# Performance work log

Measured on AMD Instinct MI355X. Metric: run time of the kernel, lower is better.

The kernel has to match this reference:

```python
import jax, jax.numpy as jnp
import numpy as np

B, C, N = 1, 128, 8192
K, KNN, RES, NUM, NUM_LEVELS, BASE_SCALE = 128, 32, 3, 27, 3, 0.25


def _prelu(x, a):
    return jnp.where(x >= 0, x, a.reshape(()) * x)


def _gn(x, gamma, beta, groups, eps=1e-5):
    b, ch = x.shape[0], x.shape[1]
    xr = x.reshape(b, groups, -1)
    mu = xr.mean(axis=2, keepdims=True)
    var = xr.var(axis=2, keepdims=True)
    xn = ((xr - mu) * jax.lax.rsqrt(var + eps)).reshape(x.shape)
    shp = (1, ch) + (1,) * (x.ndim - 2)
    return xn * gamma.reshape(shp) + beta.reshape(shp)


def _conv1x1(x, W, b):
    y = jnp.einsum('oc,bc...->bo...', W, x)
    return y + b.reshape((1, -1) + (1,) * (x.ndim - 2))


def _base():
    i = np.arange(NUM)
    return jnp.asarray(np.stack([i // 9 % 3 - 1, i // 3 % 3 - 1, i % 3 - 1], 1).astype(np.float32))


def _forward(fmap1, fmap2, xyz2, coords,
             out_w1, out_b1, out_g, out_bt, out_pr, out_w2, out_b2,
             vox_w1, vox_b1, vox_g, vox_bt, vox_pr, vox_w2, vox_b2,
             knn_w1, knn_b1, knn_g, knn_bt, knn_pr, knn_ow, knn_ob):
    b, c, n_p = fmap1.shape
    sg = jax.lax.stop_gradient
    # correlation + truncation (init_module)
    corr = jnp.einsum('bcn,bcm->bnm', fmap1, fmap2) / jnp.sqrt(jnp.asarray(c, fmap1.dtype))
    tcorr, tidx = jax.lax.top_k(corr, K)                       # (b, n_p, K)
    bi = jnp.arange(b)[:, None, None]
    ni = jnp.arange(n_p)[None, :, None]
    txyz2 = xyz2[bi, tidx]                                     # (b, n_p, K, 3)
    ones = jnp.ones_like(tcorr)

    feats = []
    # multi-level voxel average pooling (scatter_add into 27 cubes)
    for i in range(NUM_LEVELS):
        r = BASE_SCALE * 2 ** i
        dv = jnp.round((txyz2 - coords[:, :, None, :]) / r)
        valid = jnp.all(jnp.abs(dv) <= 1.0, axis=-1)
        iv = dv + 1.0
        cube = (iv[..., 0] * 9 + iv[..., 1] * 3 + iv[..., 2]).astype(jnp.int32)
        cube = sg(jnp.where(valid, cube, 0))
        vf = sg(valid.astype(tcorr.dtype))
        cadd = jnp.zeros((b, n_p, NUM), tcorr.dtype).at[bi, ni, cube].add(tcorr * vf)
        ccnt = jnp.clip(jnp.zeros((b, n_p, NUM), tcorr.dtype).at[bi, ni, cube].add(ones * vf), 1, n_p)
        feats.append((cadd / ccnt).transpose(0, 2, 1))         # (b, 27, n_p)

    # coarse level: scatter_max to find per-cube center candidates (all no-grad)
    r = BASE_SCALE * 2 ** 3
    R = 2.0 * r
    sxyz, scrd = sg(txyz2), sg(coords)
    dv = jnp.round((sxyz - scrd[:, :, None, :]) / R)
    validc = jnp.all(jnp.abs(dv) <= 1.5, axis=-1)
    cidx = ((dv[..., 0] + 1.0) * 9 + (dv[..., 1] + 1.0) * 3 + (dv[..., 2] + 1.0)).astype(jnp.int32) + 1
    cidx = jnp.where(validc, cidx, 0)                          # (b, n_p, K) in [0, 27]
    vals = sg(tcorr) * validc
    masked = jnp.where(cidx[..., None] == jnp.arange(NUM + 1), vals[..., None], -jnp.inf)
    center_corr = masked.max(axis=2)[:, :, 1:]                 # (b, n_p, 27)
    center_idx = masked.argmax(axis=2)[:, :, 1:]
    mask_oob = center_corr <= 0                                # covers empty bins (-inf)
    center_idx = jnp.where(mask_oob, 0, center_idx)
    center_coord = sxyz[bi, ni, center_idx]                    # (b, n_p, 27, 3)

    base = _base()
    lim = (R - r) / 2.0
    idx_scatter = jnp.full((b, n_p, K), NUM, jnp.int32)
    moves = []
    for k in range(NUM):                                       # fixed 27-voxel loop
        vkc = (scrd + base[k] * R)[:, :, None, :]
        mv = jnp.clip(center_coord[:, :, k:k + 1, :] - vkc, -lim, lim) + vkc
        moves.append(mv)
        rep = jnp.all(jnp.abs((sxyz - mv) / r) <= 0.5, axis=-1) & ~mask_oob[:, :, k:k + 1]
        idx_scatter = jnp.where(rep, k, idx_scatter)           # later k overwrites (torch order)
    voxel_xyz = jnp.concatenate(moves, axis=2)                 # (b, n_p, 27, 3), no-grad

    cadd = jnp.zeros((b, n_p, NUM + 1), tcorr.dtype).at[bi, ni, idx_scatter].add(tcorr)
    ccnt = jnp.zeros((b, n_p, NUM + 1), tcorr.dtype).at[bi, ni, idx_scatter].add(ones)
    voxel_corr = cadd[:, :, :NUM] / jnp.clip(ccnt[:, :, :NUM], 1, n_p)

    vin = jnp.concatenate([voxel_corr[:, None], voxel_xyz.transpose(0, 3, 1, 2)], axis=1)  # (b,4,n_p,27)
    h = _prelu(_gn(_conv1x1(vin, vox_w1, vox_b1), vox_g, vox_bt, 8), vox_pr)
    h = _conv1x1(h, vox_w2, vox_b2)                            # (b,1,n_p,27)
    feats.append(h[:, 0].transpose(0, 2, 1))                   # (b,27,n_p)

    vfeat = jnp.concatenate(feats, axis=1)                     # (b,108,n_p)
    vfeat = _prelu(_gn(_conv1x1(vfeat, out_w1, out_b1), out_g, out_bt, 8), out_pr)
    voxel_out = _conv1x1(vfeat, out_w2, out_b2)                # (b,64,n_p)

    # knn branch
    dist = jnp.sum((txyz2 - coords[:, :, None, :]) ** 2, axis=-1)
    _, nbr = jax.lax.top_k(-sg(dist), KNN)                     # (b,n_p,KNN)
    knn_corr = jnp.take_along_axis(tcorr, nbr, axis=2)[:, None]            # (b,1,n_p,KNN)
    knn_xyz = txyz2[bi, ni, nbr].transpose(0, 3, 1, 2) - coords.transpose(0, 2, 1)[:, :, :, None]
    kf = _prelu(_gn(_conv1x1(jnp.concatenate([knn_corr, knn_xyz], 1), knn_w1, knn_b1), knn_g, knn_bt, 8), knn_pr)
    kf = kf.max(axis=3)                                        # (b,64,n_p)
    return voxel_out + _conv1x1(kf, knn_ow, knn_ob)


def setup_inputs() -> dict:
    key = jax.random.key(0)
    ks = jax.random.split(key, 26)
    xyz2 = jax.random.uniform(ks[0], (B, N, 3), jnp.float32, -3.0, 3.0)
    coords = xyz2 + 0.3 * jax.random.normal(ks[1], (B, N, 3), jnp.float32)
    w = lambda k, s, sc=0.1: sc * jax.random.normal(k, s, jnp.float32)
    return {
        'fmap1': jax.random.normal(ks[2], (B, C, N), jnp.float32),
        'fmap2': jax.random.normal(ks[3], (B, C, N), jnp.float32),
        'xyz2': xyz2, 'coords': coords,
        'out_w1': w(ks[4], (128, 108)), 'out_b1': w(ks[5], (128,)),
        'out_g': 1.0 + w(ks[6], (128,), 0.05), 'out_bt': w(ks[7], (128,), 0.05),
        'out_pr': jnp.full((1,), 0.25, jnp.float32),
        'out_w2': w(ks[8], (64, 128)), 'out_b2': w(ks[9], (64,)),
        'vox_w1': w(ks[10], (32, 4)), 'vox_b1': w(ks[11], (32,)),
        'vox_g': 1.0 + w(ks[12], (32,), 0.05), 'vox_bt': w(ks[13], (32,), 0.05),
        'vox_pr': jnp.full((1,), 0.25, jnp.float32),
        'vox_w2': w(ks[14], (1, 32)), 'vox_b2': w(ks[15], (1,)),
        'knn_w1': w(ks[16], (64, 4)), 'knn_b1': w(ks[17], (64,)),
        'knn_g': 1.0 + w(ks[18], (64,), 0.05), 'knn_bt': w(ks[19], (64,), 0.05),
        'knn_pr': jnp.full((1,), 0.25, jnp.float32),
        'knn_ow': w(ks[20], (64, 64)), 'knn_ob': w(ks[21], (64,)),
    }


def reference(fmap1, fmap2, xyz2, coords,
              out_w1, out_b1, out_g, out_bt, out_pr, out_w2, out_b2,
              vox_w1, vox_b1, vox_g, vox_bt, vox_pr, vox_w2, vox_b2,
              knn_w1, knn_b1, knn_g, knn_bt, knn_pr, knn_ow, knn_ob):
    return _forward(fmap1, fmap2, xyz2, coords,
                    out_w1, out_b1, out_g, out_bt, out_pr, out_w2, out_b2,
                    vox_w1, vox_b1, vox_g, vox_bt, vox_pr, vox_w2, vox_b2,
                    knn_w1, knn_b1, knn_g, knn_bt, knn_pr, knn_ow, knn_ob)
```

## Files before the change

kernel.cpp:

```cpp
#include <hip/hip_runtime.h>
#include <math.h>

#define NPT 8192
#define CCH 128
#define KK  128

typedef __attribute__((ext_vector_type(8))) short short8;
typedef __attribute__((ext_vector_type(4))) float f32x4;

__device__ __forceinline__ unsigned f2key(float f) {
  unsigned u = __float_as_uint(f);
  return u ^ ((u & 0x80000000u) ? 0xFFFFFFFFu : 0x80000000u);
}
__device__ __forceinline__ float key2f(unsigned k) {
  unsigned u = (k & 0x80000000u) ? (k ^ 0x80000000u) : ~k;
  return __uint_as_float(u);
}

__global__ void k_zero(double* s) {
  int t = threadIdx.x;
  if (t < 76) s[t] = 0.0;
}

__global__ __launch_bounds__(256) void k_split(const float* __restrict__ src,
                                               short* __restrict__ d0,
                                               short* __restrict__ d1,
                                               short* __restrict__ d2) {
  __shared__ float tile[2048];
  int g = blockIdx.x, t = threadIdx.x;
#pragma unroll
  for (int p = 0; p < 8; ++p) {
    int i = t + p * 256;
    int c = i >> 4, m = i & 15;
    tile[i] = src[(size_t)c * NPT + g * 16 + m];
  }
  __syncthreads();
  int o = t >> 4, m = t & 15;
  short8 w0, w1, w2;
#pragma unroll
  for (int j = 0; j < 8; ++j) {
    float a = tile[(o * 8 + j) * 16 + m];
    unsigned ua = __float_as_uint(a);
    unsigned uh = ua & 0xFFFF0000u;
    float r = a - __uint_as_float(uh);
    unsigned um = __float_as_uint(r) & 0xFFFF0000u;
    float r2 = r - __uint_as_float(um);
    unsigned ul = __float_as_uint(r2) & 0xFFFF0000u;
    w0[j] = (short)(uh >> 16);
    w1[j] = (short)(um >> 16);
    w2[j] = (short)(ul >> 16);
  }
  size_t base = (((size_t)g * 16 + o) * 16 + m) * 8;
  *(short8*)(d0 + base) = w0;
  *(short8*)(d1 + base) = w1;
  *(short8*)(d2 + base) = w2;
}

#define BHALF 12288
__global__ __launch_bounds__(256) void k_gemm_mfma(
    const short* __restrict__ a0, const short* __restrict__ a1, const short* __restrict__ a2,
    const short* __restrict__ b0, const short* __restrict__ b1, const short* __restrict__ b2,
    unsigned short* __restrict__ kslab, unsigned short* __restrict__ rslab, int row0) {
  __shared__ short bl[2 * BHALF];
  int tid = threadIdx.x;
  int wv = tid >> 6, lane = tid & 63;
  int m15 = lane & 15, quad = lane >> 4;
  int rowgb = (row0 >> 4) + blockIdx.y * 8 + wv * 2;
  int colg0 = blockIdx.x * 8;
  int bu_t[6], bu_oc[6], bu_m[6], bu_split[6], bu_laddr[6];
#pragma unroll
  for (int k = 0; k < 6; ++k) {
    int u = tid + k * 256;
    bu_split[k] = u >> 9;
    int r1 = u & 511;
    bu_t[k] = r1 >> 6;
    bu_oc[k] = (r1 >> 4) & 3;
    bu_m[k] = r1 & 15;
    bu_laddr[k] = (((bu_split[k] * 8 + bu_t[k]) * 4 + bu_oc[k]) * 16 + bu_m[k]) * 8;
  }
  f32x4 acc[2][8];
#pragma unroll
  for (int rg = 0; rg < 2; ++rg)
#pragma unroll
    for (int t = 0; t < 8; ++t) acc[rg][t] = (f32x4){0.f, 0.f, 0.f, 0.f};
  {
    short8 bv[6];
#pragma unroll
    for (int k = 0; k < 6; ++k) {
      const short* bp = (bu_split[k] == 0) ? b0 : (bu_split[k] == 1) ? b1 : b2;
      size_t gaddr = (((size_t)(colg0 + bu_t[k]) * 16 + (0 * 4 + bu_oc[k])) * 16 + bu_m[k]) * 8;
      bv[k] = *(const short8*)(bp + gaddr);
    }
#pragma unroll
    for (int k = 0; k < 6; ++k) *(short8*)(bl + bu_laddr[k]) = bv[k];
  }
  __syncthreads();
#pragma unroll
  for (int s = 0; s < 4; ++s) {
    short8 bnext[6];
    if (s < 3) {
#pragma unroll
      for (int k = 0; k < 6; ++k) {
        const short* bp = (bu_split[k] == 0) ? b0 : (bu_split[k] == 1) ? b1 : b2;
        size_t gaddr =
            (((size_t)(colg0 + bu_t[k]) * 16 + ((s + 1) * 4 + bu_oc[k])) * 16 + bu_m[k]) * 8;
        bnext[k] = *(const short8*)(bp + gaddr);
      }
    }
    int oct = s * 4 + quad;
    short8 A0[2], A1[2], A2[2];
#pragma unroll
    for (int rg = 0; rg < 2; ++rg) {
      size_t ab = (((size_t)(rowgb + rg) * 16 + oct) * 16 + m15) * 8;
      A0[rg] = *(const short8*)(a0 + ab);
      A1[rg] = *(const short8*)(a1 + ab);
      A2[rg] = *(const short8*)(a2 + ab);
    }
    const short* buf = bl + (s & 1) * BHALF;
#pragma unroll
    for (int t = 0; t < 8; ++t) {
      int lb = ((t * 4 + quad) * 16 + m15) * 8;
      short8 B0 = *(const short8*)(buf + lb);
      short8 B1 = *(const short8*)(buf + 4096 + lb);
      short8 B2 = *(const short8*)(buf + 8192 + lb);
#pragma unroll
      for (int rg = 0; rg < 2; ++rg) {
        acc[rg][t] = __builtin_amdgcn_mfma_f32_16x16x32_bf16(A2[rg], B0, acc[rg][t], 0, 0, 0);
        acc[rg][t] = __builtin_amdgcn_mfma_f32_16x16x32_bf16(A0[rg], B2, acc[rg][t], 0, 0, 0);
        acc[rg][t] = __builtin_amdgcn_mfma_f32_16x16x32_bf16(A1[rg], B1, acc[rg][t], 0, 0, 0);
        acc[rg][t] = __builtin_amdgcn_mfma_f32_16x16x32_bf16(A1[rg], B0, acc[rg][t], 0, 0, 0);
        acc[rg][t] = __builtin_amdgcn_mfma_f32_16x16x32_bf16(A0[rg], B1, acc[rg][t], 0, 0, 0);
        acc[rg][t] = __builtin_amdgcn_mfma_f32_16x16x32_bf16(A0[rg], B0, acc[rg][t], 0, 0, 0);
      }
    }
    if (s < 3) {
      short* nbuf = bl + ((s + 1) & 1) * BHALF;
#pragma unroll
      for (int k = 0; k < 6; ++k) *(short8*)(nbuf + bu_laddr[k]) = bnext[k];
    }
    __syncthreads();
  }
#pragma unroll
  for (int rg = 0; rg < 2; ++rg) {
    int rl = (blockIdx.y * 8 + wv * 2 + rg) * 16 + quad * 4;
#pragma unroll
    for (int t = 0; t < 8; ++t) {
      int col = (colg0 + t) * 16 + m15;
#pragma unroll
      for (int r = 0; r < 4; ++r) {
        unsigned key = f2key(acc[rg][t][r]);
        kslab[(size_t)(rl + r) * NPT + col] = (unsigned short)(key >> 16);
        rslab[(size_t)(rl + r) * NPT + col] = (unsigned short)(key & 0xFFFFu);
      }
    }
  }
}

__global__ __launch_bounds__(256) void k_select16(const unsigned short* __restrict__ kslab,
                                                  const unsigned short* __restrict__ rslab,
                                                  int row0,
                                                  float* __restrict__ tcorr,
                                                  int* __restrict__ tidx) {
  __shared__ int wcnt[2][4];
  __shared__ int s_ntop, s_ncand;
  __shared__ unsigned candm[2048];
  const float sc = 0.08838834764831845f;
  int tid = threadIdx.x, lane = tid & 63, wv = tid >> 6;
  int rl = blockIdx.x, row = row0 + rl;
  const unsigned* rp = (const unsigned*)(kslab + (size_t)rl * NPT);
  const unsigned short* rr = rslab + (size_t)rl * NPT;
  unsigned k16[32];
#pragma unroll
  for (int j = 0; j < 16; ++j) {
    unsigned p = rp[tid + j * 256];
    k16[2 * j] = p & 0xFFFFu;
    k16[2 * j + 1] = p >> 16;
  }
  if (tid == 0) { s_ntop = 0; s_ncand = 0; }
  unsigned P = 0;
  int par = 0;
#pragma unroll 1
  for (int b = 15; b >= 0; --b) {
    unsigned T = P | (1u << b);
    int c = 0;
#pragma unroll
    for (int j = 0; j < 32; ++j) c += (k16[j] >= T) ? 1 : 0;
    for (int off = 32; off; off >>= 1) c += __shfl_down(c, off);
    if (lane == 0) wcnt[par][wv] = c;
    __syncthreads();
    int tot = wcnt[par][0] + wcnt[par][1] + wcnt[par][2] + wcnt[par][3];
    if (tot >= KK) P = T;
    par ^= 1;
  }
  int base = row * KK;
#pragma unroll
  for (int j = 0; j < 32; ++j) {
    unsigned kh = k16[j];
    int col = (tid + (j >> 1) * 256) * 2 + (j & 1);
    if (kh > P) {
      int p = atomicAdd(&s_ntop, 1);
      unsigned k32 = (kh << 16) | (unsigned)rr[col];
      tcorr[base + p] = key2f(k32) * sc;
      tidx[base + p] = col;
    } else if (kh == P) {
      int c = atomicAdd(&s_ncand, 1);
      if (c < 2048) candm[c] = (((unsigned)rr[col]) << 13) | (unsigned)(8191 - col);
    }
  }
  __syncthreads();
  int ntop = s_ntop;
  int nc = s_ncand < 2048 ? s_ncand : 2048;
  int krem = KK - ntop;
  for (int ci = tid; ci < nc; ci += 256) {
    unsigned mi = candm[ci];
    int r = 0;
    for (int j = 0; j < nc; ++j) r += (candm[j] > mi) ? 1 : 0;
    if (r < krem) {
      unsigned res = mi >> 13;
      int col = 8191 - (int)(mi & 0x1FFFu);
      unsigned k32 = (P << 16) | res;
      tcorr[base + ntop + r] = key2f(k32) * sc;
      tidx[base + ntop + r] = col;
    }
  }
}

__global__ __launch_bounds__(128) void k_point(const float* __restrict__ tcorr,
                                               const int* __restrict__ tidx,
                                               const float* __restrict__ xyz2,
                                               const float* __restrict__ coords,
                                               float* __restrict__ feats,
                                               float* __restrict__ vox_in,
                                               float* __restrict__ knn_in) {
  __shared__ float px[128], py[128], pz[128];
  __shared__ float4 dd4s[32];
  __shared__ float cadd[81], ccnt[81];
  __shared__ unsigned long long cmax[27];
  __shared__ unsigned long long gmax;
  __shared__ float4 mvp[27];
  __shared__ float vadd[28];
  __shared__ int vcnt[28];
  int n = blockIdx.x, t = threadIdx.x;
  float v = tcorr[(size_t)n * KK + t];
  int idx = tidx[(size_t)n * KK + t];
  float p0 = xyz2[idx * 3 + 0], p1 = xyz2[idx * 3 + 1], p2 = xyz2[idx * 3 + 2];
  float c0 = coords[n * 3 + 0], c1 = coords[n * 3 + 1], c2 = coords[n * 3 + 2];
  px[t] = p0; py[t] = p1; pz[t] = p2;
  float dx = p0 - c0, dy = p1 - c1, dz = p2 - c2;
  float d = dx * dx + dy * dy + dz * dz;
  ((float*)dd4s)[t] = d;
  if (t < 81) { cadd[t] = 0.f; ccnt[t] = 0.f; }
  if (t < 27) cmax[t] = 0ULL;
  if (t < 28) { vadd[t] = 0.f; vcnt[t] = 0; }
  if (t == 0) gmax = 0ULL;
  __syncthreads();
#pragma unroll
  for (int lvl = 0; lvl < 3; ++lvl) {
    float rinv = (lvl == 0) ? 4.f : (lvl == 1) ? 2.f : 1.f;
    float d0 = rintf(dx * rinv), d1 = rintf(dy * rinv), d2 = rintf(dz * rinv);
    if (fabsf(d0) <= 1.f && fabsf(d1) <= 1.f && fabsf(d2) <= 1.f) {
      int cube = (int)(d0 + 1.f) * 9 + (int)(d1 + 1.f) * 3 + (int)(d2 + 1.f);
      atomicAdd(&cadd[lvl * 27 + cube], v);
      atomicAdd(&ccnt[lvl * 27 + cube], 1.f);
    }
  }
  unsigned long long pk = (((unsigned long long)f2key(v)) << 32) | (unsigned)t;
  atomicMax(&gmax, pk);
  {
    float d0 = rintf(dx * 0.25f), d1 = rintf(dy * 0.25f), d2 = rintf(dz * 0.25f);
    if (fabsf(d0) <= 1.5f && fabsf(d1) <= 1.5f && fabsf(d2) <= 1.5f) {
      int bin = (int)(d0 + 1.f) * 9 + (int)(d1 + 1.f) * 3 + (int)(d2 + 1.f);
      atomicMax(&cmax[bin], pk);
    }
  }
  __syncthreads();
  if (t < 27) {
    unsigned long long pkb = cmax[t];
    unsigned hi = (unsigned)(pkb >> 32);
    int ob = (hi <= 0x80000000u) ? 1 : 0;
    int ki = ob ? (int)(gmax & 0xFFFFFFFFULL) : (int)(pkb & 0xFFFFFFFFULL);
    float ccx = px[ki], ccy = py[ki], ccz = pz[ki];
    float bx = (float)(t / 9 - 1), by = (float)((t / 3) % 3 - 1), bz = (float)(t % 3 - 1);
    float vk0 = c0 + bx * 4.f, vk1 = c1 + by * 4.f, vk2 = c2 + bz * 4.f;
    float m0 = fminf(fmaxf(ccx - vk0, -1.f), 1.f) + vk0;
    float m1 = fminf(fmaxf(ccy - vk1, -1.f), 1.f) + vk1;
    float m2 = fminf(fmaxf(ccz - vk2, -1.f), 1.f) + vk2;
    mvp[t] = make_float4(m0, m1, m2, ob ? 1.f : 0.f);
    float* vp = vox_in + ((size_t)n * 27 + t) * 4;
    vp[1] = m0; vp[2] = m1; vp[3] = m2;
  }
  __syncthreads();
  int is = 27;
#pragma unroll 1
  for (int b = 0; b < 27; ++b) {
    float4 mv = mvp[b];
    if (mv.w == 0.f && fabsf(p0 - mv.x) <= 1.f && fabsf(p1 - mv.y) <= 1.f &&
        fabsf(p2 - mv.z) <= 1.f)
      is = b;
  }
  atomicAdd(&vadd[is], v);
  atomicAdd(&vcnt[is], 1);
  __syncthreads();
  if (t < 27) {
    float cnt = fmaxf((float)vcnt[t], 1.f);
    vox_in[((size_t)n * 27 + t) * 4 + 0] = vadd[t] / cnt;
  }
  if (t < 81) {
    float cnt = fminf(fmaxf(ccnt[t], 1.f), 8192.f);
    feats[(size_t)t * NPT + n] = cadd[t] / cnt;
  }
  int rank = 0;
#pragma unroll 4
  for (int j4 = 0; j4 < 32; ++j4) {
    float4 dj = dd4s[j4];
    int jb = j4 * 4;
    rank += (dj.x < d || (dj.x == d && jb + 0 < t)) ? 1 : 0;
    rank += (dj.y < d || (dj.y == d && jb + 1 < t)) ? 1 : 0;
    rank += (dj.z < d || (dj.z == d && jb + 2 < t)) ? 1 : 0;
    rank += (dj.w < d || (dj.w == d && jb + 3 < t)) ? 1 : 0;
  }
  if (rank < 32) {
    float* kp = knn_in + ((size_t)n * 32 + rank) * 4;
    *(float4*)kp = make_float4(v, dx, dy, dz);
  }
}

__global__ __launch_bounds__(256) void k_moments(const float* __restrict__ vox_in,
                                                 const float* __restrict__ knn_in,
                                                 double* __restrict__ mom) {
  int b = blockIdx.x, t = threadIdx.x;
  int isknn = (b >= 256) ? 1 : 0;
  const float* src = isknn ? knn_in : vox_in;
  int nsite = isknn ? NPT * 32 : NPT * 27;
  int base = isknn ? 14 : 0;
  int bb = isknn ? b - 256 : b;
  float S0 = 0, S1 = 0, S2 = 0, S3 = 0;
  float M00 = 0, M01 = 0, M02 = 0, M03 = 0, M11 = 0, M12 = 0, M13 = 0, M22 = 0, M23 = 0, M33 = 0;
  for (int s = bb * 256 + t; s < nsite; s += 256 * 256) {
    float4 x = *(const float4*)(src + (size_t)s * 4);
    S0 += x.x; S1 += x.y; S2 += x.z; S3 += x.w;
    M00 += x.x * x.x; M01 += x.x * x.y; M02 += x.x * x.z; M03 += x.x * x.w;
    M11 += x.y * x.y; M12 += x.y * x.z; M13 += x.y * x.w;
    M22 += x.z * x.z; M23 += x.z * x.w; M33 += x.w * x.w;
  }
  float vals[14] = {S0, S1, S2, S3, M00, M01, M02, M03, M11, M12, M13, M22, M23, M33};
  for (int off = 32; off; off >>= 1)
#pragma unroll
    for (int i = 0; i < 14; ++i) vals[i] += __shfl_down(vals[i], off);
  __shared__ float part[14];
  if (t < 14) part[t] = 0.f;
  __syncthreads();
  if ((t & 63) == 0)
#pragma unroll
    for (int i = 0; i < 14; ++i) atomicAdd(&part[i], vals[i]);
  __syncthreads();
  if (t < 14) atomicAdd(&mom[base + t], (double)part[t]);
}

__device__ __forceinline__ void group_stats(const double* m, const float* W, const float* Bi,
                                            double N, int per, int g,
                                            float* mean_out, float* rstd_out) {
  double S0 = m[0], S1 = m[1], S2 = m[2], S3 = m[3];
  double M00 = m[4], M01 = m[5], M02 = m[6], M03 = m[7];
  double M11 = m[8], M12 = m[9], M13 = m[10], M22 = m[11], M23 = m[12], M33 = m[13];
  double sum = 0.0, ssq = 0.0;
  for (int k = 0; k < per; ++k) {
    int oc = g * per + k;
    double w0 = W[oc * 4 + 0], w1 = W[oc * 4 + 1], w2 = W[oc * 4 + 2], w3 = W[oc * 4 + 3];
    double b = Bi[oc];
    double ws = w0 * S0 + w1 * S1 + w2 * S2 + w3 * S3;
    double q = w0 * w0 * M00 + w1 * w1 * M11 + w2 * w2 * M22 + w3 * w3 * M33 +
               2.0 * (w0 * w1 * M01 + w0 * w2 * M02 + w0 * w3 * M03 +
                      w1 * w2 * M12 + w1 * w3 * M13 + w2 * w3 * M23);
    sum += ws + N * b;
    ssq += q + 2.0 * b * ws + N * b * b;
  }
  double cnt = N * (double)per;
  double mm = sum / cnt;
  double var = ssq / cnt - mm * mm;
  *mean_out = (float)mm;
  *rstd_out = (float)(1.0 / sqrt(var + 1e-5));
}

__global__ __launch_bounds__(256) void k_vox_apply(const float* __restrict__ vox_in,
                                                   const float* __restrict__ w1,
                                                   const float* __restrict__ b1,
                                                   const float* __restrict__ gamma,
                                                   const float* __restrict__ beta,
                                                   const float* __restrict__ pr,
                                                   const float* __restrict__ w2,
                                                   const float* __restrict__ b2,
                                                   const double* __restrict__ mom,
                                                   float* __restrict__ feats) {
  int s = blockIdx.x * 256 + threadIdx.x;
  if (s >= NPT * 27) return;
  float mean[8], rstd[8];
#pragma unroll
  for (int g = 0; g < 8; ++g)
    group_stats(mom, w1, b1, (double)NPT * 27.0, 4, g, &mean[g], &rstd[g]);
  float a = pr[0];
  float4 in = *(const float4*)(vox_in + (size_t)s * 4);
  float out = b2[0];
#pragma unroll
  for (int oc = 0; oc < 32; ++oc) {
    float4 w = *(const float4*)(w1 + oc * 4);
    float h = w.x * in.x + w.y * in.y + w.z * in.z + w.w * in.w + b1[oc];
    int g = oc >> 2;
    float xn = (h - mean[g]) * rstd[g] * gamma[oc] + beta[oc];
    float y = (xn >= 0.f) ? xn : a * xn;
    out += w2[oc] * y;
  }
  int n = s / 27, bb = s - n * 27;
  feats[(size_t)(81 + bb) * NPT + n] = out;
}

__global__ __launch_bounds__(256) void k_knn_max(const float* __restrict__ knn_in,
                                                 const float* __restrict__ w1,
                                                 const float* __restrict__ b1,
                                                 const float* __restrict__ gamma,
                                                 const float* __restrict__ beta,
                                                 const float* __restrict__ pr,
                                                 const double* __restrict__ mom,
                                                 float* __restrict__ kf) {
  int tid0 = blockIdx.x * 256 + threadIdx.x;
  int n = tid0 & (NPT - 1);
  int oc = tid0 >> 13;
  float mean, rstd;
  group_stats(mom, w1, b1, (double)NPT * 32.0, 8, oc >> 3, &mean, &rstd);
  float4 w = *(const float4*)(w1 + oc * 4);
  float bb = b1[oc], ga = gamma[oc], be = beta[oc], a = pr[0];
  float mx = -INFINITY;
  for (int j = 0; j < 32; ++j) {
    float4 in = *(const float4*)(knn_in + ((size_t)n * 32 + j) * 4);
    float h = w.x * in.x + w.y * in.y + w.z * in.z + w.w * in.w + bb;
    float xn = (h - mean) * rstd * ga + be;
    float y = (xn >= 0.f) ? xn : a * xn;
    mx = fmaxf(mx, y);
  }
  kf[(size_t)oc * NPT + n] = mx;
}

__global__ __launch_bounds__(256) void k_out1(const float* __restrict__ feats,
                                              const float* __restrict__ w1,
                                              const float* __restrict__ b1,
                                              float* __restrict__ h1,
                                              double* __restrict__ stats) {
  __shared__ float wlds[108 * 16];
  __shared__ float ls, lq;
  int t = threadIdx.x;
  int ocb = blockIdx.y * 16;
  for (int i = t; i < 108 * 16; i += 256) {
    int j = i / 108, ic = i - j * 108;
    wlds[ic * 16 + j] = w1[ocb * 108 + i];
  }
  if (t == 0) { ls = 0.f; lq = 0.f; }
  __syncthreads();
  int n = blockIdx.x * 256 + t;
  float acc[16];
#pragma unroll
  for (int j = 0; j < 16; ++j) acc[j] = b1[ocb + j];
#pragma unroll 4
  for (int ic = 0; ic < 108; ++ic) {
    float v = feats[(size_t)ic * NPT + n];
    const float4* w4 = (const float4*)(wlds + ic * 16);
#pragma unroll
    for (int q = 0; q < 4; ++q) {
      float4 w = w4[q];
      acc[q * 4 + 0] += w.x * v; acc[q * 4 + 1] += w.y * v;
      acc[q * 4 + 2] += w.z * v; acc[q * 4 + 3] += w.w * v;
    }
  }
  float s = 0.f, q = 0.f;
#pragma unroll
  for (int j = 0; j < 16; ++j) {
    h1[(size_t)(ocb + j) * NPT + n] = acc[j];
    s += acc[j]; q += acc[j] * acc[j];
  }
  for (int off = 32; off; off >>= 1) { s += __shfl_down(s, off); q += __shfl_down(q, off); }
  if ((t & 63) == 0) { atomicAdd(&ls, s); atomicAdd(&lq, q); }
  __syncthreads();
  if (t == 0) {
    atomicAdd(&stats[2 * blockIdx.y + 0], (double)ls);
    atomicAdd(&stats[2 * blockIdx.y + 1], (double)lq);
  }
}

__global__ __launch_bounds__(256) void k_final(const float* __restrict__ h1,
                                               const float* __restrict__ kf,
                                               const float* __restrict__ gamma,
                                               const float* __restrict__ beta,
                                               const float* __restrict__ pr,
                                               const float* __restrict__ w2,
                                               const float* __restrict__ b2,
                                               const float* __restrict__ kow,
                                               const float* __restrict__ kob,
                                               const double* __restrict__ stats,
                                               float* __restrict__ out) {
  __shared__ float wl[192 * 8];
  __shared__ float scl[128], sft[128];
  int t = threadIdx.x;
  int ocb = blockIdx.y * 8;
  for (int i = t; i < 128 * 8; i += 256) {
    int j = i >> 7, ic = i & 127;
    wl[ic * 8 + j] = w2[(ocb + j) * 128 + ic];
  }
  for (int i = t; i < 64 * 8; i += 256) {
    int j = i >> 6, ic = i & 63;
    wl[(128 + ic) * 8 + j] = kow[(ocb + j) * 64 + ic];
  }
  if (t < 128) {
    const double cntd = 16.0 * 8192.0;
    int g = t >> 4;
    double m = stats[2 * g] / cntd;
    double var = stats[2 * g + 1] / cntd - m * m;
    float rs = (float)(1.0 / sqrt(var + 1e-5));
    float ga = gamma[t];
    scl[t] = rs * ga;
    sft[t] = beta[t] - (float)m * rs * ga;
  }
  __syncthreads();
  int n = blockIdx.x * 256 + t;
  float a = pr[0];
  float acc[8];
#pragma unroll
  for (int j = 0; j < 8; ++j) acc[j] = b2[ocb + j] + kob[ocb + j];
#pragma unroll 2
  for (int ic = 0; ic < 128; ++ic) {
    float x = h1[(size_t)ic * NPT + n];
    float xn = x * scl[ic] + sft[ic];
    float y = (xn >= 0.f) ? xn : a * xn;
    const float4* w4 = (const float4*)(wl + ic * 8);
    float4 wa = w4[0], wb = w4[1];
    acc[0] += wa.x * y; acc[1] += wa.y * y; acc[2] += wa.z * y; acc[3] += wa.w * y;
    acc[4] += wb.x * y; acc[5] += wb.y * y; acc[6] += wb.z * y; acc[7] += wb.w * y;
  }
#pragma unroll 2
  for (int ic = 0; ic < 64; ++ic) {
    float y = kf[(size_t)ic * NPT + n];
    const float4* w4 = (const float4*)(wl + (128 + ic) * 8);
    float4 wa = w4[0], wb = w4[1];
    acc[0] += wa.x * y; acc[1] += wa.y * y; acc[2] += wa.z * y; acc[3] += wa.w * y;
    acc[4] += wb.x * y; acc[5] += wb.y * y; acc[6] += wb.z * y; acc[7] += wb.w * y;
  }
#pragma unroll
  for (int j = 0; j < 8; ++j)
    out[(size_t)(ocb + j) * NPT + n] = acc[j];
}

extern "C" void kernel_launch(void* const* d_in, const int* in_sizes, int n_in,
                              void* d_out, int out_size, void* d_ws, size_t ws_size,
                              hipStream_t stream) {
  (void)in_sizes; (void)n_in; (void)out_size;
  const float* fmap1  = (const float*)d_in[0];
  const float* fmap2  = (const float*)d_in[1];
  const float* xyz2   = (const float*)d_in[2];
  const float* coords = (const float*)d_in[3];
  const float* out_w1 = (const float*)d_in[4];
  const float* out_b1 = (const float*)d_in[5];
  const float* out_g  = (const float*)d_in[6];
  const float* out_bt = (const float*)d_in[7];
  const float* out_pr = (const float*)d_in[8];
  const float* out_w2 = (const float*)d_in[9];
  const float* out_b2 = (const float*)d_in[10];
  const float* vox_w1 = (const float*)d_in[11];
  const float* vox_b1 = (const float*)d_in[12];
  const float* vox_g  = (const float*)d_in[13];
  const float* vox_bt = (const float*)d_in[14];
  const float* vox_pr = (const float*)d_in[15];
  const float* vox_w2 = (const float*)d_in[16];
  const float* vox_b2 = (const float*)d_in[17];
  const float* knn_w1 = (const float*)d_in[18];
  const float* knn_b1 = (const float*)d_in[19];
  const float* knn_g  = (const float*)d_in[20];
  const float* knn_bt = (const float*)d_in[21];
  const float* knn_pr = (const float*)d_in[22];
  const float* knn_ow = (const float*)d_in[23];
  const float* knn_ob = (const float*)d_in[24];

  float* ws = (float*)d_ws;
  const size_t nonslab = 9633944ull;
  int SR;
  if (ws_size >= (67108864ull + nonslab) * 4ull + 4096ull) SR = 8192;
  else if (ws_size >= (33554432ull + nonslab) * 4ull + 4096ull) SR = 4096;
  else if (ws_size >= (16777216ull + nonslab) * 4ull + 4096ull) SR = 2048;
  else if (ws_size >= (8388608ull + nonslab) * 4ull + 4096ull) SR = 1024;
  else SR = 512;

  unsigned short* kslab = (unsigned short*)ws;
  unsigned short* rslab = kslab + (size_t)SR * NPT;
  float* after  = ws + (size_t)SR * NPT;
  float* tcorr  = after;
  int*   tidx   = (int*)(tcorr + (size_t)NPT * KK);
  float* feats  = tcorr + (size_t)NPT * KK * 2;
  float* vox_in = feats + 108 * NPT;
  float* knn_in = vox_in + (size_t)NPT * 27 * 4;
  float* h1     = knn_in + (size_t)NPT * 32 * 4;
  float* kf     = h1 + 128 * NPT;
  double* stats = (double*)(kf + 64 * NPT);
  double* mom   = stats + 48;
  short* a0s    = (short*)(mom + 28);
  short* a1s    = a0s + (size_t)NPT * CCH;
  short* a2s    = a1s + (size_t)NPT * CCH;
  short* b0s    = a2s + (size_t)NPT * CCH;
  short* b1s    = b0s + (size_t)NPT * CCH;
  short* b2s    = b1s + (size_t)NPT * CCH;

  hipLaunchKernelGGL(k_zero, dim3(1), dim3(128), 0, stream, stats);
  hipLaunchKernelGGL(k_split, dim3(NPT / 16), dim3(256), 0, stream, fmap1, a0s, a1s, a2s);
  hipLaunchKernelGGL(k_split, dim3(NPT / 16), dim3(256), 0, stream, fmap2, b0s, b1s, b2s);
  int iters = NPT / SR;
  for (int s = 0; s < iters; ++s) {
    hipLaunchKernelGGL(k_gemm_mfma, dim3(NPT / 128, SR / 128), dim3(256), 0, stream,
                       a0s, a1s, a2s, b0s, b1s, b2s, kslab, rslab, s * SR);
    hipLaunchKernelGGL(k_select16, dim3(SR), dim3(256), 0, stream, kslab, rslab, s * SR,
                       tcorr, tidx);
  }
  hipLaunchKernelGGL(k_point, dim3(NPT), dim3(128), 0, stream, tcorr, tidx, xyz2, coords,
                     feats, vox_in, knn_in);
  hipLaunchKernelGGL(k_moments, dim3(512), dim3(256), 0, stream, vox_in, knn_in, mom);
  hipLaunchKernelGGL(k_vox_apply, dim3((NPT * 27 + 255) / 256), dim3(256), 0, stream, vox_in,
                     vox_w1, vox_b1, vox_g, vox_bt, vox_pr, vox_w2, vox_b2, mom, feats);
  hipLaunchKernelGGL(k_knn_max, dim3(64 * NPT / 256), dim3(256), 0, stream, knn_in, knn_w1,
                     knn_b1, knn_g, knn_bt, knn_pr, mom + 14, kf);
  hipLaunchKernelGGL(k_out1, dim3(NPT / 256, 8), dim3(256), 0, stream, feats, out_w1, out_b1, h1,
                     stats + 32);
  hipLaunchKernelGGL(k_final, dim3(NPT / 256, 8), dim3(256), 0, stream, h1, kf, out_g, out_bt,
                     out_pr, out_w2, out_b2, knn_ow, knn_ob, stats + 32, (float*)d_out);
}
```

Measured before the change: 491.5 us.

## Prefetch GEMM A fragments, shorten select radix loop, precompute group-norm scale/shift

The MFMA GEMM now loads the next k-slice of A fragments into registers during the current slice's compute instead of at its start, hiding global load latency. The top-k selection stops the radix bisection three bits early, widens the candidate buffer, and packs the low key bits into the candidate word, with a fallback that finishes the bisection when candidates overflow. A new single-block kernel computes the per-channel group-norm scale and shift once, so the vox and knn kernels no longer recompute double-precision group statistics in every thread. This costs extra registers in the GEMM and adds a small kernel launch.

New measurement: 535.1 us. 8.9% more time.

```diff
diff --git a/kernel.cpp b/kernel.cpp
--- a/kernel.cpp
+++ b/kernel.cpp
@@ -88,16 +88,25 @@
 #pragma unroll
     for (int k = 0; k < 6; ++k) {
       const short* bp = (bu_split[k] == 0) ? b0 : (bu_split[k] == 1) ? b1 : b2;
-      size_t gaddr = (((size_t)(colg0 + bu_t[k]) * 16 + (0 * 4 + bu_oc[k])) * 16 + bu_m[k]) * 8;
+      size_t gaddr = (((size_t)(colg0 + bu_t[k]) * 16 + bu_oc[k]) * 16 + bu_m[k]) * 8;
       bv[k] = *(const short8*)(bp + gaddr);
     }
 #pragma unroll
     for (int k = 0; k < 6; ++k) *(short8*)(bl + bu_laddr[k]) = bv[k];
+  }
+  short8 A0[2], A1[2], A2[2];
+#pragma unroll
+  for (int rg = 0; rg < 2; ++rg) {
+    size_t ab = (((size_t)(rowgb + rg) * 16 + quad) * 16 + m15) * 8;
+    A0[rg] = *(const short8*)(a0 + ab);
+    A1[rg] = *(const short8*)(a1 + ab);
+    A2[rg] = *(const short8*)(a2 + ab);
   }
   __syncthreads();
 #pragma unroll
   for (int s = 0; s < 4; ++s) {
     short8 bnext[6];
+    short8 A0n[2], A1n[2], A2n[2];
     if (s < 3) {
 #pragma unroll
       for (int k = 0; k < 6; ++k) {
@@ -106,15 +115,14 @@
             (((size_t)(colg0 + bu_t[k]) * 16 + ((s + 1) * 4 + bu_oc[k])) * 16 + bu_m[k]) * 8;
         bnext[k] = *(const short8*)(bp + gaddr);
       }
-    }
-    int oct = s * 4 + quad;
-    short8 A0[2], A1[2], A2[2];
-#pragma unroll
-    for (int rg = 0; rg < 2; ++rg) {
-      size_t ab = (((size_t)(rowgb + rg) * 16 + oct) * 16 + m15) * 8;
-      A0[rg] = *(const short8*)(a0 + ab);
-      A1[rg] = *(const short8*)(a1 + ab);
-      A2[rg] = *(const short8*)(a2 + ab);
+      int octn = (s + 1) * 4 + quad;
+#pragma unroll
+      for (int rg = 0; rg < 2; ++rg) {
+        size_t ab = (((size_t)(rowgb + rg) * 16 + octn) * 16 + m15) * 8;
+        A0n[rg] = *(const short8*)(a0 + ab);
+        A1n[rg] = *(const short8*)(a1 + ab);
+        A2n[rg] = *(const short8*)(a2 + ab);
+      }
     }
     const short* buf = bl + (s & 1) * BHALF;
 #pragma unroll
@@ -137,6 +145,10 @@
       short* nbuf = bl + ((s + 1) & 1) * BHALF;
 #pragma unroll
       for (int k = 0; k < 6; ++k) *(short8*)(nbuf + bu_laddr[k]) = bnext[k];
+#pragma unroll
+      for (int rg = 0; rg < 2; ++rg) {
+        A0[rg] = A0n[rg]; A1[rg] = A1n[rg]; A2[rg] = A2n[rg];
+      }
     }
     __syncthreads();
   }
@@ -156,6 +168,7 @@
   }
 }
 
+#define SCAP 3072
 __global__ __launch_bounds__(256) void k_select16(const unsigned short* __restrict__ kslab,
                                                   const unsigned short* __restrict__ rslab,
                                                   int row0,
@@ -163,7 +176,7 @@
                                                   int* __restrict__ tidx) {
   __shared__ int wcnt[2][4];
   __shared__ int s_ntop, s_ncand;
-  __shared__ unsigned candm[2048];
+  __shared__ unsigned candm[SCAP];
   const float sc = 0.08838834764831845f;
   int tid = threadIdx.x, lane = tid & 63, wv = tid >> 6;
   int rl = blockIdx.x, row = row0 + rl;
@@ -180,7 +193,7 @@
   unsigned P = 0;
   int par = 0;
 #pragma unroll 1
-  for (int b = 15; b >= 0; --b) {
+  for (int b = 15; b >= 3; --b) {
     unsigned T = P | (1u << b);
     int c = 0;
 #pragma unroll
@@ -192,35 +205,77 @@
     if (tot >= KK) P = T;
     par ^= 1;
   }
+  unsigned binp = P >> 3;
   int base = row * KK;
 #pragma unroll
   for (int j = 0; j < 32; ++j) {
     unsigned kh = k16[j];
     int col = (tid + (j >> 1) * 256) * 2 + (j & 1);
-    if (kh > P) {
+    if ((kh >> 3) > binp) {
       int p = atomicAdd(&s_ntop, 1);
       unsigned k32 = (kh << 16) | (unsigned)rr[col];
       tcorr[base + p] = key2f(k32) * sc;
       tidx[base + p] = col;
-    } else if (kh == P) {
+    } else if ((kh >> 3) == binp) {
       int c = atomicAdd(&s_ncand, 1);
-      if (c < 2048) candm[c] = (((unsigned)rr[col]) << 13) | (unsigned)(8191 - col);
+      if (c < SCAP)
+        candm[c] = ((kh & 7u) << 29) | (((unsigned)rr[col]) << 13) | (unsigned)(8191 - col);
     }
   }
   __syncthreads();
   int ntop = s_ntop;
-  int nc = s_ncand < 2048 ? s_ncand : 2048;
+  int nc = s_ncand;
   int krem = KK - ntop;
-  for (int ci = tid; ci < nc; ci += 256) {
-    unsigned mi = candm[ci];
-    int r = 0;
-    for (int j = 0; j < nc; ++j) r += (candm[j] > mi) ? 1 : 0;
-    if (r < krem) {
-      unsigned res = mi >> 13;
-      int col = 8191 - (int)(mi & 0x1FFFu);
-      unsigned k32 = (P << 16) | res;
-      tcorr[base + ntop + r] = key2f(k32) * sc;
-      tidx[base + ntop + r] = col;
+  if (nc <= SCAP) {
+    for (int ci = tid; ci < nc; ci += 256) {
+      unsigned mi = candm[ci];
+      int r = 0;
+      for (int j = 0; j < nc; ++j) r += (candm[j] > mi) ? 1 : 0;
+      if (r < krem) {
+        unsigned k32 = ((P | (mi >> 29)) << 16) | ((mi >> 13) & 0xFFFFu);
+        int col = 8191 - (int)(mi & 0x1FFFu);
+        tcorr[base + ntop + r] = key2f(k32) * sc;
+        tidx[base + ntop + r] = col;
+      }
+    }
+  } else {
+#pragma unroll 1
+    for (int b = 2; b >= 0; --b) {
+      unsigned T = P | (1u << b);
+      int c = 0;
+#pragma unroll
+      for (int j = 0; j < 32; ++j) c += (k16[j] >= T) ? 1 : 0;
+      for (int off = 32; off; off >>= 1) c += __shfl_down(c, off);
+      if (lane == 0) wcnt[par][wv] = c;
+      __syncthreads();
+      int tot = wcnt[par][0] + wcnt[par][1] + wcnt[par][2] + wcnt[par][3];
+      if (tot >= KK) P = T;
+      par ^= 1;
+    }
+#pragma unroll
+    for (int j = 0; j < 32; ++j) {
+      unsigned kh = k16[j];
+      int col = (tid + (j >> 1) * 256) * 2 + (j & 1);
+      if ((kh >> 3) == binp && kh > P) {
+        int p = atomicAdd(&s_ntop, 1);
+        unsigned k32 = (kh << 16) | (unsigned)rr[col];
+        tcorr[base + p] = key2f(k32) * sc;
+        tidx[base + p] = col;
+      }
+    }
+    __syncthreads();
+#pragma unroll
+    for (int j = 0; j < 32; ++j) {
+      unsigned kh = k16[j];
+      int col = (tid + (j >> 1) * 256) * 2 + (j & 1);
+      if (kh == P) {
+        int p = atomicAdd(&s_ntop, 1);
+        if (p < KK) {
+          unsigned k32 = (kh << 16) | (unsigned)rr[col];
+          tcorr[base + p] = key2f(k32) * sc;
+          tidx[base + p] = col;
+        }
+      }
     }
   }
 }
@@ -382,22 +437,39 @@
   *rstd_out = (float)(1.0 / sqrt(var + 1e-5));
 }
 
+__global__ void k_scale(const double* __restrict__ mom,
+                        const float* __restrict__ vw1, const float* __restrict__ vb1,
+                        const float* __restrict__ vg, const float* __restrict__ vbt,
+                        const float* __restrict__ kw1, const float* __restrict__ kb1,
+                        const float* __restrict__ kg, const float* __restrict__ kbt,
+                        float* __restrict__ sb) {
+  int t = threadIdx.x;
+  if (t < 32) {
+    float mean, rstd;
+    group_stats(mom, vw1, vb1, (double)NPT * 27.0, 4, t >> 2, &mean, &rstd);
+    float ga = vg[t];
+    sb[t] = rstd * ga;
+    sb[32 + t] = vbt[t] - mean * rstd * ga;
+  } else if (t < 96) {
+    int oc = t - 32;
+    float mean, rstd;
+    group_stats(mom + 14, kw1, kb1, (double)NPT * 32.0, 8, oc >> 3, &mean, &rstd);
+    float ga = kg[oc];
+    sb[64 + oc] = rstd * ga;
+    sb[128 + oc] = kbt[oc] - mean * rstd * ga;
+  }
+}
+
 __global__ __launch_bounds__(256) void k_vox_apply(const float* __restrict__ vox_in,
                                                    const float* __restrict__ w1,
                                                    const float* __restrict__ b1,
-                                                   const float* __restrict__ gamma,
-                                                   const float* __restrict__ beta,
                                                    const float* __restrict__ pr,
                                                    const float* __restrict__ w2,
                                                    const float* __restrict__ b2,
-                                                   const double* __restrict__ mom,
+                                                   const float* __restrict__ sb,
                                                    float* __restrict__ feats) {
   int s = blockIdx.x * 256 + threadIdx.x;
   if (s >= NPT * 27) return;
-  float mean[8], rstd[8];
-#pragma unroll
-  for (int g = 0; g < 8; ++g)
-    group_stats(mom, w1, b1, (double)NPT * 27.0, 4, g, &mean[g], &rstd[g]);
   float a = pr[0];
   float4 in = *(const float4*)(vox_in + (size_t)s * 4);
   float out = b2[0];
@@ -405,8 +477,7 @@
   for (int oc = 0; oc < 32; ++oc) {
     float4 w = *(const float4*)(w1 + oc * 4);
     float h = w.x * in.x + w.y * in.y + w.z * in.z + w.w * in.w + b1[oc];
-    int g = oc >> 2;
-    float xn = (h - mean[g]) * rstd[g] * gamma[oc] + beta[oc];
+    float xn = h * sb[oc] + sb[32 + oc];
     float y = (xn >= 0.f) ? xn : a * xn;
     out += w2[oc] * y;
   }
@@ -417,23 +488,20 @@
 __global__ __launch_bounds__(256) void k_knn_max(const float* __restrict__ knn_in,
                                                  const float* __restrict__ w1,
                                                  const float* __restrict__ b1,
-                                                 const float* __restrict__ gamma,
-                                                 const float* __restrict__ beta,
                                                  const float* __restrict__ pr,
-                                                 const double* __restrict__ mom,
+                                                 const float* __restrict__ sb,
                                                  float* __restrict__ kf) {
   int tid0 = blockIdx.x * 256 + threadIdx.x;
   int n = tid0 & (NPT - 1);
   int oc = tid0 >> 13;
-  float mean, rstd;
-  group_stats(mom, w1, b1, (double)NPT * 32.0, 8, oc >> 3, &mean, &rstd);
+  float scl = sb[64 + oc], sft = sb[128 + oc];
   float4 w = *(const float4*)(w1 + oc * 4);
-  float bb = b1[oc], ga = gamma[oc], be = beta[oc], a = pr[0];
+  float bb = b1[oc], a = pr[0];
   float mx = -INFINITY;
   for (int j = 0; j < 32; ++j) {
     float4 in = *(const float4*)(knn_in + ((size_t)n * 32 + j) * 4);
     float h = w.x * in.x + w.y * in.y + w.z * in.z + w.w * in.w + bb;
-    float xn = (h - mean) * rstd * ga + be;
+    float xn = h * scl + sft;
     float y = (xn >= 0.f) ? xn : a * xn;
     mx = fmaxf(mx, y);
   }
@@ -578,7 +646,7 @@
   const float* knn_ob = (const float*)d_in[24];
 
   float* ws = (float*)d_ws;
-  const size_t nonslab = 9633944ull;
+  const size_t nonslab = 9634136ull;
   int SR;
   if (ws_size >= (67108864ull + nonslab) * 4ull + 4096ull) SR = 8192;
   else if (ws_size >= (33554432ull + nonslab) * 4ull + 4096ull) SR = 4096;
@@ -598,7 +666,8 @@
   float* kf     = h1 + 128 * NPT;
   double* stats = (double*)(kf + 64 * NPT);
   double* mom   = stats + 48;
-  short* a0s    = (short*)(mom + 28);
+  float* sb     = (float*)(mom + 28);
+  short* a0s    = (short*)(sb + 192);
   short* a1s    = a0s + (size_t)NPT * CCH;
   short* a2s    = a1s + (size_t)NPT * CCH;
   short* b0s    = a2s + (size_t)NPT * CCH;
@@ -618,10 +687,12 @@
   hipLaunchKernelGGL(k_point, dim3(NPT), dim3(128), 0, stream, tcorr, tidx, xyz2, coords,
                      feats, vox_in, knn_in);
   hipLaunchKernelGGL(k_moments, dim3(512), dim3(256), 0, stream, vox_in, knn_in, mom);
+  hipLaunchKernelGGL(k_scale, dim3(1), dim3(128), 0, stream, mom, vox_w1, vox_b1, vox_g, vox_bt,
+                     knn_w1, knn_b1, knn_g, knn_bt, sb);
   hipLaunchKernelGGL(k_vox_apply, dim3((NPT * 27 + 255) / 256), dim3(256), 0, stream, vox_in,
-                     vox_w1, vox_b1, vox_g, vox_bt, vox_pr, vox_w2, vox_b2, mom, feats);
+                     vox_w1, vox_b1, vox_pr, vox_w2, vox_b2, sb, feats);
   hipLaunchKernelGGL(k_knn_max, dim3(64 * NPT / 256), dim3(256), 0, stream, knn_in, knn_w1,
-                     knn_b1, knn_g, knn_bt, knn_pr, mom + 14, kf);
+                     knn_b1, knn_pr, sb, kf);
   hipLaunchKernelGGL(k_out1, dim3(NPT / 256, 8), dim3(256), 0, stream, feats, out_w1, out_b1, h1,
                      stats + 32);
   hipLaunchKernelGGL(k_final, dim3(NPT / 256, 8), dim3(256), 0, stream, h1, kf, out_g, out_bt,
```
